# Performance work log

Measured on AMD Instinct MI355X. Metric: run time of the kernel, lower is better.

Reference implementation:

```python
import jax, jax.numpy as jnp
import numpy as np

N, E, G, T, H, ED, IN_D, OUT_D = 50000, 1600000, 64, 5, 64, 9, 10, 3
EPS = 1e-6

def _seg_mean(vals, seg, num):
    s = jax.ops.segment_sum(vals, seg, num_segments=num)
    c = jax.ops.segment_sum(jnp.ones((vals.shape[0],), vals.dtype), seg, num_segments=num)
    return s / jnp.maximum(c, 1.0)[:, None], c

def per_graph_edge_norm(edge_attr, edge_graph, num_graphs):
    # standardize each edge-feature column per graph (zero-shot transfer trick)
    mu, _ = _seg_mean(edge_attr, edge_graph, num_graphs)
    sq, _ = _seg_mean(edge_attr * edge_attr, edge_graph, num_graphs)
    var = jnp.maximum(sq - mu * mu, 0.0)
    std = jnp.sqrt(var)
    return (edge_attr - mu[edge_graph]) / (std[edge_graph] + EPS)

def setup_inputs() -> dict:
    key = jax.random.key(0)
    ks = jax.random.split(key, 24)
    s = 0.05  # weight scale to keep ReLU chains stable
    inp = {
        'x': jax.random.normal(ks[0], (N, IN_D), jnp.float32),
        'edge_index': jax.random.randint(ks[1], (2, E), 0, N),
        'edge_attr': jax.random.normal(ks[2], (E, ED), jnp.float32),
        'batch': jnp.sort(jax.random.randint(ks[3], (N,), 0, G)),
        'lift_W1': jax.random.normal(ks[4], (IN_D, H), jnp.float32) * s,
        'lift_b1': jnp.zeros((H,), jnp.float32),
        'lift_W2': jax.random.normal(ks[5], (H, H), jnp.float32) * s,
        'lift_b2': jnp.zeros((H,), jnp.float32),
        'Wself': jax.random.normal(ks[6], (T, H, H), jnp.float32) * s,
        'bself': jnp.zeros((T, H), jnp.float32),
        'msg_W0': jax.random.normal(ks[7], (T, H + ED, H), jnp.float32) * s,
        'msg_b0': jnp.zeros((T, H), jnp.float32),
        'msg_W1': jax.random.normal(ks[8], (T, H, H), jnp.float32) * s,
        'msg_b1': jnp.zeros((T, H), jnp.float32),
        'msg_W2': jax.random.normal(ks[9], (T, H, H), jnp.float32) * s,
        'msg_b2': jnp.zeros((T, H), jnp.float32),
        'gate_W': jax.random.normal(ks[10], (T, 1, H), jnp.float32) * s,
        'gate_b': jnp.zeros((T, H), jnp.float32),
        'proj_W1': jax.random.normal(ks[11], (H, H), jnp.float32) * s,
        'proj_b1': jnp.zeros((H,), jnp.float32),
        'proj_W2': jax.random.normal(ks[12], (H, OUT_D), jnp.float32) * s,
        'proj_b2': jnp.zeros((OUT_D,), jnp.float32),
    }
    return inp

def _gno(x, edge_index, edge_attr, batch,
         lift_W1, lift_b1, lift_W2, lift_b2,
         Wself, bself, msg_W0, msg_b0, msg_W1, msg_b1, msg_W2, msg_b2,
         gate_W, gate_b, proj_W1, proj_b1, proj_W2, proj_b2):
    src, dst = edge_index[0], edge_index[1]
    edge_graph = batch[src]
    ea = per_graph_edge_norm(edge_attr, edge_graph, G)  # cols 0:9 == all cols
    log_diag_y = x[:, 4:5]                               # [N,1]
    v0 = jax.nn.relu(x @ lift_W1 + lift_b1) @ lift_W2 + lift_b2  # lift
    v = v0
    for t in range(T):
        # gather -> per-edge MLP -> scatter-mean (AdmittanceKernelLayer)
        h = jnp.concatenate([v[src], ea], axis=-1)              # [E, H+ED]
        h = jax.nn.relu(h @ msg_W0[t] + msg_b0[t])
        h = jax.nn.relu(h @ msg_W1[t] + msg_b1[t])
        m = h @ msg_W2[t] + msg_b2[t]                           # [E, H]
        agg, _ = _seg_mean(m, dst, N)                           # mean aggregation
        gate = jax.nn.sigmoid(log_diag_y @ gate_W[t] + gate_b[t])  # [N,H]
        v = jax.nn.relu(v @ Wself[t] + bself[t] + agg + v0) * gate
        # dropout inactive at inference
    out = jax.nn.relu(v @ proj_W1 + proj_b1) @ proj_W2 + proj_b2  # project
    return out

def reference(x, edge_index, edge_attr, batch,
              lift_W1, lift_b1, lift_W2, lift_b2,
              Wself, bself, msg_W0, msg_b0, msg_W1, msg_b1, msg_W2, msg_b2,
              gate_W, gate_b, proj_W1, proj_b1, proj_W2, proj_b2):
    return _gno(x, edge_index, edge_attr, batch,
                lift_W1, lift_b1, lift_W2, lift_b2,
                Wself, bself, msg_W0, msg_b0, msg_W1, msg_b1, msg_W2, msg_b2,
                gate_W, gate_b, proj_W1, proj_b1, proj_W2, proj_b2)
```

## Files before the change

### kernel.cpp

```cpp
#include <hip/hip_runtime.h>
#include <math.h>

#define NN 50000
#define NE 1600000
#define NG 64
#define NT 5
#define NH 64
#define NED 9
#define NIN 10
#define NOUT 3
#define EPSF 1e-6f
#define NSUB (NE / 16)

typedef __attribute__((ext_vector_type(8))) short s8v;
typedef __attribute__((ext_vector_type(4))) short s4v;
typedef __attribute__((ext_vector_type(4))) float f32x4;

__device__ __forceinline__ unsigned short f2bf(float f) {
    union { float f; unsigned int u; } v; v.f = f;
    unsigned int r = v.u + 0x7FFFu + ((v.u >> 16) & 1u);
    return (unsigned short)(r >> 16);
}
__device__ __forceinline__ float bf2f(unsigned short b) {
    union { unsigned int u; float f; } v; v.u = ((unsigned int)b) << 16;
    return v.f;
}

__global__ void stats_kernel(const int* __restrict__ ei, const float* __restrict__ ea,
                             const int* __restrict__ batch,
                             float* __restrict__ ssum, float* __restrict__ ssq,
                             float* __restrict__ scnt, int* __restrict__ ecnt) {
    __shared__ float lsum[NG * NED];
    __shared__ float lsq[NG * NED];
    __shared__ float lcnt[NG];
    for (int i = threadIdx.x; i < NG * NED; i += blockDim.x) { lsum[i] = 0.f; lsq[i] = 0.f; }
    for (int i = threadIdx.x; i < NG; i += blockDim.x) lcnt[i] = 0.f;
    __syncthreads();
    int lane = threadIdx.x & 63;
    int stride = gridDim.x * blockDim.x;
    for (int e = blockIdx.x * blockDim.x + threadIdx.x; e < NE; e += stride) {
        int s = ei[e];
        int g = batch[s];
        atomicAdd(&ecnt[ei[NE + e]], 1);
        float a[NED];
#pragma unroll
        for (int d = 0; d < NED; ++d) a[d] = ea[(size_t)e * NED + d];
        int g0 = __builtin_amdgcn_readfirstlane(g);
        if (__all(g == g0)) {
            float sv[NED], qv[NED];
#pragma unroll
            for (int d = 0; d < NED; ++d) { sv[d] = a[d]; qv[d] = a[d] * a[d]; }
#pragma unroll
            for (int off = 32; off; off >>= 1) {
#pragma unroll
                for (int d = 0; d < NED; ++d) {
                    sv[d] += __shfl_down(sv[d], off);
                    qv[d] += __shfl_down(qv[d], off);
                }
            }
            if (lane == 0) {
#pragma unroll
                for (int d = 0; d < NED; ++d) {
                    atomicAdd(&lsum[g0 * NED + d], sv[d]);
                    atomicAdd(&lsq[g0 * NED + d], qv[d]);
                }
                atomicAdd(&lcnt[g0], 64.f);
            }
        } else {
            atomicAdd(&lcnt[g], 1.0f);
#pragma unroll
            for (int d = 0; d < NED; ++d) {
                atomicAdd(&lsum[g * NED + d], a[d]);
                atomicAdd(&lsq[g * NED + d], a[d] * a[d]);
            }
        }
    }
    __syncthreads();
    for (int i = threadIdx.x; i < NG * NED; i += blockDim.x) {
        atomicAdd(&ssum[i], lsum[i]);
        atomicAdd(&ssq[i], lsq[i]);
    }
    for (int i = threadIdx.x; i < NG; i += blockDim.x) atomicAdd(&scnt[i], lcnt[i]);
}

__global__ void stats_fin(const float* __restrict__ ssum, const float* __restrict__ ssq,
                          const float* __restrict__ scnt,
                          float* __restrict__ mu, float* __restrict__ rstd) {
    int i = blockIdx.x * blockDim.x + threadIdx.x;
    if (i >= NG * NED) return;
    int g = i / NED;
    float c = fmaxf(scnt[g], 1.0f);
    float m = ssum[i] / c;
    float q = ssq[i] / c;
    float var = fmaxf(q - m * m, 0.f);
    mu[i] = m;
    rstd[i] = 1.0f / (sqrtf(var) + EPSF);
}

__global__ void scan1_kernel(const int* __restrict__ ecnt, int* __restrict__ partial) {
    __shared__ int sm[256];
    int i = blockIdx.x * 256 + threadIdx.x;
    sm[threadIdx.x] = (i < NN) ? ecnt[i] : 0;
    __syncthreads();
    for (int off = 128; off; off >>= 1) {
        if (threadIdx.x < off) sm[threadIdx.x] += sm[threadIdx.x + off];
        __syncthreads();
    }
    if (threadIdx.x == 0) partial[blockIdx.x] = sm[0];
}
__global__ void scan2_kernel(int* __restrict__ partial, int nb) {
    __shared__ int sm[256];
    int t = threadIdx.x;
    sm[t] = (t < nb) ? partial[t] : 0;
    __syncthreads();
    for (int off = 1; off < 256; off <<= 1) {
        int v = (t >= off) ? sm[t - off] : 0;
        __syncthreads();
        sm[t] += v;
        __syncthreads();
    }
    if (t < nb) partial[t] = (t ? sm[t - 1] : 0);
}
__global__ void scan3_kernel(const int* __restrict__ ecnt, const int* __restrict__ partial,
                             int* __restrict__ offs) {
    __shared__ int sm[256];
    int b = blockIdx.x, t = threadIdx.x, i = b * 256 + t;
    int x = (i < NN) ? ecnt[i] : 0;
    sm[t] = x;
    __syncthreads();
    for (int off = 1; off < 256; off <<= 1) {
        int v = (t >= off) ? sm[t - off] : 0;
        __syncthreads();
        sm[t] += v;
        __syncthreads();
    }
    if (i < NN) offs[i] = sm[t] - x + partial[b];
}

__global__ void permute_kernel(const int* __restrict__ ei, const int* __restrict__ offs,
                               int* __restrict__ cursor, int* __restrict__ perm) {
    int stride = gridDim.x * blockDim.x;
    for (int e = blockIdx.x * blockDim.x + threadIdx.x; e < NE; e += stride) {
        int d = ei[NE + e];
        int pos = offs[d] + atomicAdd(&cursor[d], 1);
        perm[pos] = e;
    }
}

__global__ void pack_kernel(const int* __restrict__ perm, const int* __restrict__ ei,
                            const float* __restrict__ ea, const int* __restrict__ batch,
                            const float* __restrict__ mu, const float* __restrict__ rstd,
                            int* __restrict__ srcPerm, int* __restrict__ dstPerm,
                            unsigned short* __restrict__ eaN) {
    int stride = gridDim.x * blockDim.x;
    for (int p = blockIdx.x * blockDim.x + threadIdx.x; p < NE; p += stride) {
        int e = perm[p];
        int s = ei[e], d = ei[NE + e];
        int g = batch[s];
        srcPerm[p] = s;
        dstPerm[p] = d;
#pragma unroll
        for (int k = 0; k < NED; ++k) {
            float val = (ea[(size_t)e * NED + k] - mu[g * NED + k]) * rstd[g * NED + k];
            eaN[(size_t)k * NE + p] = f2bf(val);
        }
    }
}

__global__ __launch_bounds__(256) void lift_kernel(
    const float* __restrict__ x,
    const float* __restrict__ W1, const float* __restrict__ b1,
    const float* __restrict__ W2, const float* __restrict__ b2,
    float* __restrict__ v0, float* __restrict__ v, float* __restrict__ ldy) {
    __shared__ float sW1[NIN * NH];
    __shared__ __align__(16) float sW2[NH][NH];
    __shared__ float sb1[NH], sb2[NH];
    for (int i = threadIdx.x; i < NIN * NH; i += blockDim.x) sW1[i] = W1[i];
    for (int i = threadIdx.x; i < NH * NH; i += blockDim.x) {
        int k = i >> 6, j = i & 63;
        sW2[j][k] = W2[i];
    }
    for (int i = threadIdx.x; i < NH; i += blockDim.x) { sb1[i] = b1[i]; sb2[i] = b2[i]; }
    __syncthreads();
    int stride = gridDim.x * blockDim.x;
    for (int n = blockIdx.x * blockDim.x + threadIdx.x; n < NN; n += stride) {
        float xr[NIN];
#pragma unroll
        for (int k = 0; k < NIN; ++k) xr[k] = x[(size_t)n * NIN + k];
        ldy[n] = xr[4];
        float h[NH];
#pragma unroll
        for (int j = 0; j < NH; ++j) {
            float acc = sb1[j];
#pragma unroll
            for (int k = 0; k < NIN; ++k) acc += xr[k] * sW1[k * NH + j];
            h[j] = fmaxf(acc, 0.f);
        }
#pragma unroll
        for (int j = 0; j < NH; ++j) {
            float acc = sb2[j];
#pragma unroll
            for (int k = 0; k < NH; k += 4) {
                float4 w = *(const float4*)&sW2[j][k];
                acc += h[k] * w.x + h[k + 1] * w.y + h[k + 2] * w.z + h[k + 3] * w.w;
            }
            v0[(size_t)n * NH + j] = acc;
            v[(size_t)n * NH + j] = acc;
        }
    }
}

__device__ __forceinline__ void gemm_acc68(const float* __restrict__ Ab,
                                           const float* __restrict__ Wb,
                                           int K, int te, int tj, float acc[4][4]) {
#pragma unroll 4
    for (int k = 0; k < K; ++k) {
        float4 a = *(const float4*)(Ab + k * 68 + (te << 2));
        float4 b = *(const float4*)(Wb + (k << 6) + (tj << 2));
        acc[0][0] = fmaf(a.x, b.x, acc[0][0]);
        acc[0][1] = fmaf(a.x, b.y, acc[0][1]);
        acc[0][2] = fmaf(a.x, b.z, acc[0][2]);
        acc[0][3] = fmaf(a.x, b.w, acc[0][3]);
        acc[1][0] = fmaf(a.y, b.x, acc[1][0]);
        acc[1][1] = fmaf(a.y, b.y, acc[1][1]);
        acc[1][2] = fmaf(a.y, b.z, acc[1][2]);
        acc[1][3] = fmaf(a.y, b.w, acc[1][3]);
        acc[2][0] = fmaf(a.z, b.x, acc[2][0]);
        acc[2][1] = fmaf(a.z, b.y, acc[2][1]);
        acc[2][2] = fmaf(a.z, b.z, acc[2][2]);
        acc[2][3] = fmaf(a.z, b.w, acc[2][3]);
        acc[3][0] = fmaf(a.w, b.x, acc[3][0]);
        acc[3][1] = fmaf(a.w, b.y, acc[3][1]);
        acc[3][2] = fmaf(a.w, b.z, acc[3][2]);
        acc[3][3] = fmaf(a.w, b.w, acc[3][3]);
    }
}

__global__ __launch_bounds__(256, 4) void u_kernel(
    const float* __restrict__ v, const float* __restrict__ W0v,
    const float* __restrict__ b0, float* __restrict__ U) {
    __shared__ __align__(16) float Vt[64][68];
    __shared__ __align__(16) float sW[64][64];
    __shared__ float sb[64];
    const int tid = threadIdx.x;
    const int base = blockIdx.x * 64;
    const int te = tid >> 4, tj = tid & 15;

    {
        int r = tid >> 2;
        int kb = (tid & 3) << 4;
        int n = base + r;
        const float4* vrow = (const float4*)(v + (size_t)n * NH + kb);
#pragma unroll
        for (int q = 0; q < 4; ++q) {
            float4 f = (n < NN) ? vrow[q] : make_float4(0.f, 0.f, 0.f, 0.f);
            int k = kb + q * 4;
            Vt[k + 0][r] = f.x; Vt[k + 1][r] = f.y; Vt[k + 2][r] = f.z; Vt[k + 3][r] = f.w;
        }
    }
    for (int i4 = tid; i4 < 64 * 16; i4 += 256) {
        int k = i4 >> 4, c4 = i4 & 15;
        *(float4*)&sW[k][c4 * 4] = *(const float4*)(W0v + (size_t)k * 64 + c4 * 4);
    }
    if (tid < 64) sb[tid] = b0[tid];
    __syncthreads();

    float acc[4][4];
    {
        float b0_ = sb[tj * 4 + 0], b1_ = sb[tj * 4 + 1], b2_ = sb[tj * 4 + 2], b3_ = sb[tj * 4 + 3];
#pragma unroll
        for (int ee = 0; ee < 4; ++ee) { acc[ee][0] = b0_; acc[ee][1] = b1_; acc[ee][2] = b2_; acc[ee][3] = b3_; }
    }
    gemm_acc68(&Vt[0][0], &sW[0][0], 64, te, tj, acc);

#pragma unroll
    for (int ee = 0; ee < 4; ++ee) {
        int n = base + te * 4 + ee;
        if (n < NN)
            *(float4*)&U[(size_t)n * NH + tj * 4] =
                make_float4(acc[ee][0], acc[ee][1], acc[ee][2], acc[ee][3]);
    }
}

__global__ __launch_bounds__(256, 4) void edge4_kernel(
    const int* __restrict__ srcPerm, const int* __restrict__ dstPerm,
    const unsigned short* __restrict__ eaN,
    const float* __restrict__ W0e, const float* __restrict__ W1, const float* __restrict__ b1,
    const float* __restrict__ U, float* __restrict__ nodesum) {
    __shared__ __align__(16) float sWe[NED][64];
    __shared__ __align__(16) short W1frag[8][64][8];
    __shared__ __align__(16) short h0bf[4][16 * 64];
    __shared__ __align__(16) float h1s[4][16 * 64];
    __shared__ int sDstS[4][16];

    const int tid = threadIdx.x;
    const int lane = tid & 63, w = tid >> 6;
    const int l15 = lane & 15, l4 = lane >> 4;

    for (int i4 = tid; i4 < NED * 16; i4 += 256) {
        int k = i4 >> 4, c4 = i4 & 15;
        *(float4*)&sWe[k][c4 * 4] = *(const float4*)(W0e + (size_t)k * 64 + c4 * 4);
    }
    for (int idx = tid; idx < 2 * 4 * 64; idx += 256) {
        int kc = idx >> 8, c = (idx >> 6) & 3, ln = idx & 63;
        int fl15 = ln & 15, fl4 = ln >> 4;
        int col = 16 * c + fl15;
        s8v frag;
#pragma unroll
        for (int j = 0; j < 8; ++j) {
            int k = kc * 32 + fl4 * 8 + j;
            frag[j] = (short)f2bf(W1[(size_t)k * 64 + col]);
        }
        *(s8v*)&W1frag[kc * 4 + c][ln][0] = frag;
    }
    float b1r[4];
#pragma unroll
    for (int c = 0; c < 4; ++c) b1r[c] = b1[16 * c + l15];
    __syncthreads();

    short* myh0 = h0bf[w];
    float* myh1 = h1s[w];
    int*   myd  = sDstS[w];
    const int gw = blockIdx.x * 4 + w;
    const int nw = gridDim.x * 4;

    for (int st = gw; st < NSUB; st += nw) {
        const int e16 = st * 16;
        if (lane < 16) myd[lane] = dstPerm[e16 + lane];

        int4 s4 = *(const int4*)(srcPerm + e16 + 4 * l4);
        ushort4 eu[NED];
#pragma unroll
        for (int d = 0; d < NED; ++d)
            eu[d] = *(const ushort4*)(eaN + (size_t)d * NE + e16 + 4 * l4);

        float acc0[4][4];
        {
            const int* sp = (const int*)&s4;
#pragma unroll
            for (int ee = 0; ee < 4; ++ee) {
                float4 u4 = *(const float4*)(U + (size_t)sp[ee] * NH + 4 * l15);
                acc0[ee][0] = u4.x; acc0[ee][1] = u4.y; acc0[ee][2] = u4.z; acc0[ee][3] = u4.w;
            }
        }
#pragma unroll
        for (int d = 0; d < NED; ++d) {
            float4 wv = *(const float4*)&sWe[d][4 * l15];
            float a0 = bf2f((unsigned short)eu[d].x), a1 = bf2f((unsigned short)eu[d].y);
            float a2 = bf2f((unsigned short)eu[d].z), a3 = bf2f((unsigned short)eu[d].w);
            acc0[0][0] = fmaf(a0, wv.x, acc0[0][0]); acc0[0][1] = fmaf(a0, wv.y, acc0[0][1]);
            acc0[0][2] = fmaf(a0, wv.z, acc0[0][2]); acc0[0][3] = fmaf(a0, wv.w, acc0[0][3]);
            acc0[1][0] = fmaf(a1, wv.x, acc0[1][0]); acc0[1][1] = fmaf(a1, wv.y, acc0[1][1]);
            acc0[1][2] = fmaf(a1, wv.z, acc0[1][2]); acc0[1][3] = fmaf(a1, wv.w, acc0[1][3]);
            acc0[2][0] = fmaf(a2, wv.x, acc0[2][0]); acc0[2][1] = fmaf(a2, wv.y, acc0[2][1]);
            acc0[2][2] = fmaf(a2, wv.z, acc0[2][2]); acc0[2][3] = fmaf(a2, wv.w, acc0[2][3]);
            acc0[3][0] = fmaf(a3, wv.x, acc0[3][0]); acc0[3][1] = fmaf(a3, wv.y, acc0[3][1]);
            acc0[3][2] = fmaf(a3, wv.z, acc0[3][2]); acc0[3][3] = fmaf(a3, wv.w, acc0[3][3]);
        }

#pragma unroll
        for (int ee = 0; ee < 4; ++ee) {
            int row = 4 * l4 + ee;
            s4v p;
            p[0] = (short)f2bf(fmaxf(acc0[ee][0], 0.f));
            p[1] = (short)f2bf(fmaxf(acc0[ee][1], 0.f));
            p[2] = (short)f2bf(fmaxf(acc0[ee][2], 0.f));
            p[3] = (short)f2bf(fmaxf(acc0[ee][3], 0.f));
            *(s4v*)((char*)myh0 + row * 128 + ((l15 * 8) ^ ((row & 7) << 4))) = p;
        }

        f32x4 acc[4];
#pragma unroll
        for (int c = 0; c < 4; ++c) {
            float b = b1r[c];
            acc[c][0] = b; acc[c][1] = b; acc[c][2] = b; acc[c][3] = b;
        }
        {
            const char* abase = (const char*)myh0 + l15 * 128;
            const int aswz = (l15 & 7) << 4;
#pragma unroll
            for (int kc = 0; kc < 2; ++kc) {
                s8v af = *(const s8v*)(abase + ((l4 * 16 + kc * 64) ^ aswz));
#pragma unroll
                for (int c = 0; c < 4; ++c) {
                    s8v bf = *(const s8v*)&W1frag[kc * 4 + c][lane][0];
                    acc[c] = __builtin_amdgcn_mfma_f32_16x16x32_bf16(af, bf, acc[c], 0, 0, 0);
                }
            }
        }

        int dFirst = myd[0];
        int dLast = myd[15];
        if (dFirst == dLast) {
#pragma unroll
            for (int c = 0; c < 4; ++c) {
                float vs = fmaxf(acc[c][0], 0.f) + fmaxf(acc[c][1], 0.f) +
                           fmaxf(acc[c][2], 0.f) + fmaxf(acc[c][3], 0.f);
                vs += __shfl_xor(vs, 16);
                vs += __shfl_xor(vs, 32);
                if (l4 == 0)
                    atomicAdd(&nodesum[(size_t)dFirst * NH + 16 * c + l15], vs);
            }
        } else {
#pragma unroll
            for (int r = 0; r < 4; ++r) {
                int row = 4 * l4 + r;
#pragma unroll
                for (int c = 0; c < 4; ++c)
                    myh1[row * 64 + ((16 * c + l15) ^ (l4 * 8))] = fmaxf(acc[c][r], 0.f);
            }
            int cur = dFirst;
            float a = myh1[lane];
#pragma unroll
            for (int i = 1; i < 16; ++i) {
                int dn = myd[i];
                float hv = myh1[i * 64 + (lane ^ ((i >> 2) * 8))];
                if (dn != cur) {
                    atomicAdd(&nodesum[(size_t)cur * NH + lane], a);
                    cur = dn;
                    a = hv;
                } else {
                    a += hv;
                }
            }
            atomicAdd(&nodesum[(size_t)cur * NH + lane], a);
        }
    }
}

__global__ __launch_bounds__(256, 2) void update3_kernel(
    const float* __restrict__ Wself, const float* __restrict__ bself,
    const float* __restrict__ W2, const float* __restrict__ b2,
    const float* __restrict__ gWt, const float* __restrict__ gbt,
    const float* __restrict__ v0, const float* __restrict__ ldy,
    const int* __restrict__ ecnt, const float* __restrict__ nodesum,
    float* __restrict__ v) {
    __shared__ __align__(16) float Vt[64][68];
    __shared__ __align__(16) float St[64][68];
    __shared__ __align__(16) float sWs[64][64];
    __shared__ __align__(16) float sW2[64][64];
    __shared__ float sbs[64], sb2[64], sgw[64], sgb[64];
    const int tid = threadIdx.x;
    const int base = blockIdx.x * 64;
    const int te = tid >> 4, tj = tid & 15;

    {
        int r = tid >> 2;
        int kb = (tid & 3) << 4;
        int n = base + r;
        const float4* vrow = (const float4*)(v + (size_t)n * NH + kb);
        const float4* srow = (const float4*)(nodesum + (size_t)n * NH + kb);
#pragma unroll
        for (int q = 0; q < 4; ++q) {
            float4 f = (n < NN) ? vrow[q] : make_float4(0.f, 0.f, 0.f, 0.f);
            float4 g = (n < NN) ? srow[q] : make_float4(0.f, 0.f, 0.f, 0.f);
            int k = kb + q * 4;
            Vt[k + 0][r] = f.x; Vt[k + 1][r] = f.y; Vt[k + 2][r] = f.z; Vt[k + 3][r] = f.w;
            St[k + 0][r] = g.x; St[k + 1][r] = g.y; St[k + 2][r] = g.z; St[k + 3][r] = g.w;
        }
    }
    for (int i4 = tid; i4 < 64 * 16; i4 += 256) {
        int k = i4 >> 4, c4 = i4 & 15;
        *(float4*)&sWs[k][c4 * 4] = *(const float4*)(Wself + (size_t)k * 64 + c4 * 4);
        *(float4*)&sW2[k][c4 * 4] = *(const float4*)(W2 + (size_t)k * 64 + c4 * 4);
    }
    if (tid < 64) { sbs[tid] = bself[tid]; sb2[tid] = b2[tid]; sgw[tid] = gWt[tid]; sgb[tid] = gbt[tid]; }
    __syncthreads();

    float acc1[4][4], acc2[4][4];
    {
        float b0_ = sbs[tj * 4 + 0], b1_ = sbs[tj * 4 + 1], b2_ = sbs[tj * 4 + 2], b3_ = sbs[tj * 4 + 3];
#pragma unroll
        for (int ee = 0; ee < 4; ++ee) {
            acc1[ee][0] = b0_; acc1[ee][1] = b1_; acc1[ee][2] = b2_; acc1[ee][3] = b3_;
            acc2[ee][0] = 0.f; acc2[ee][1] = 0.f; acc2[ee][2] = 0.f; acc2[ee][3] = 0.f;
        }
    }
    gemm_acc68(&Vt[0][0], &sWs[0][0], 64, te, tj, acc1);
    gemm_acc68(&St[0][0], &sW2[0][0], 64, te, tj, acc2);

    float gw0 = sgw[tj * 4 + 0], gw1 = sgw[tj * 4 + 1], gw2 = sgw[tj * 4 + 2], gw3 = sgw[tj * 4 + 3];
    float gb0 = sgb[tj * 4 + 0], gb1 = sgb[tj * 4 + 1], gb2 = sgb[tj * 4 + 2], gb3 = sgb[tj * 4 + 3];
    float bb0 = sb2[tj * 4 + 0], bb1 = sb2[tj * 4 + 1], bb2 = sb2[tj * 4 + 2], bb3 = sb2[tj * 4 + 3];
#pragma unroll
    for (int ee = 0; ee < 4; ++ee) {
        int n = base + te * 4 + ee;
        if (n >= NN) continue;
        float cnt = (float)ecnt[n];
        float has = (cnt > 0.5f) ? 1.f : 0.f;
        float dninv = has / fmaxf(cnt, 1.f);
        float ld = ldy[n];
        float4 v0r = *(const float4*)&v0[(size_t)n * NH + tj * 4];
        float z0 = acc1[ee][0] + acc2[ee][0] * dninv + bb0 * has + v0r.x;
        float z1 = acc1[ee][1] + acc2[ee][1] * dninv + bb1 * has + v0r.y;
        float z2 = acc1[ee][2] + acc2[ee][2] * dninv + bb2 * has + v0r.z;
        float z3 = acc1[ee][3] + acc2[ee][3] * dninv + bb3 * has + v0r.w;
        float g0 = 1.f / (1.f + expf(-(ld * gw0 + gb0)));
        float g1 = 1.f / (1.f + expf(-(ld * gw1 + gb1)));
        float g2 = 1.f / (1.f + expf(-(ld * gw2 + gb2)));
        float g3 = 1.f / (1.f + expf(-(ld * gw3 + gb3)));
        *(float4*)&v[(size_t)n * NH + tj * 4] =
            make_float4(fmaxf(z0, 0.f) * g0, fmaxf(z1, 0.f) * g1,
                        fmaxf(z2, 0.f) * g2, fmaxf(z3, 0.f) * g3);
    }
}

__global__ __launch_bounds__(256) void proj_kernel(
    const float* __restrict__ v,
    const float* __restrict__ pW1, const float* __restrict__ pb1,
    const float* __restrict__ pW2, const float* __restrict__ pb2,
    float* __restrict__ out) {
    __shared__ __align__(16) float sW1[NH][NH];
    __shared__ float sb1[NH];
    __shared__ float sW2[NH * NOUT];
    __shared__ float sb2[NOUT];
    for (int i = threadIdx.x; i < NH * NH; i += blockDim.x) {
        int k = i >> 6, j = i & 63;
        sW1[j][k] = pW1[i];
    }
    for (int i = threadIdx.x; i < NH; i += blockDim.x) sb1[i] = pb1[i];
    for (int i = threadIdx.x; i < NH * NOUT; i += blockDim.x) sW2[i] = pW2[i];
    for (int i = threadIdx.x; i < NOUT; i += blockDim.x) sb2[i] = pb2[i];
    __syncthreads();
    int stride = gridDim.x * blockDim.x;
    for (int n = blockIdx.x * blockDim.x + threadIdx.x; n < NN; n += stride) {
        float vr[NH];
        const float4* vp = (const float4*)(v + (size_t)n * NH);
#pragma unroll
        for (int q = 0; q < NH / 4; ++q) {
            float4 f = vp[q];
            vr[4 * q + 0] = f.x; vr[4 * q + 1] = f.y; vr[4 * q + 2] = f.z; vr[4 * q + 3] = f.w;
        }
        float o0 = sb2[0], o1 = sb2[1], o2 = sb2[2];
#pragma unroll
        for (int j = 0; j < NH; ++j) {
            float acc = sb1[j];
#pragma unroll
            for (int k = 0; k < NH; k += 4) {
                float4 w = *(const float4*)&sW1[j][k];
                acc += vr[k] * w.x + vr[k + 1] * w.y + vr[k + 2] * w.z + vr[k + 3] * w.w;
            }
            float h = fmaxf(acc, 0.f);
            o0 += h * sW2[j * NOUT + 0];
            o1 += h * sW2[j * NOUT + 1];
            o2 += h * sW2[j * NOUT + 2];
        }
        out[(size_t)n * NOUT + 0] = o0;
        out[(size_t)n * NOUT + 1] = o1;
        out[(size_t)n * NOUT + 2] = o2;
    }
}

extern "C" void kernel_launch(void* const* d_in, const int* in_sizes, int n_in,
                              void* d_out, int out_size, void* d_ws, size_t ws_size,
                              hipStream_t stream) {
    (void)in_sizes; (void)n_in; (void)out_size; (void)ws_size;
    const float* x     = (const float*)d_in[0];
    const int*   ei    = (const int*)d_in[1];
    const float* ea    = (const float*)d_in[2];
    const int*   batch = (const int*)d_in[3];
    const float* lW1   = (const float*)d_in[4];
    const float* lb1   = (const float*)d_in[5];
    const float* lW2   = (const float*)d_in[6];
    const float* lb2   = (const float*)d_in[7];
    const float* Wself = (const float*)d_in[8];
    const float* bself = (const float*)d_in[9];
    const float* mW0   = (const float*)d_in[10];
    const float* mb0   = (const float*)d_in[11];
    const float* mW1   = (const float*)d_in[12];
    const float* mb1   = (const float*)d_in[13];
    const float* mW2   = (const float*)d_in[14];
    const float* mb2   = (const float*)d_in[15];
    const float* gW    = (const float*)d_in[16];
    const float* gb    = (const float*)d_in[17];
    const float* pW1   = (const float*)d_in[18];
    const float* pb1   = (const float*)d_in[19];
    const float* pW2   = (const float*)d_in[20];
    const float* pb2   = (const float*)d_in[21];
    float* out = (float*)d_out;
    float* ws  = (float*)d_ws;

    float* nodesum = ws;
    float* v0   = nodesum + (size_t)NN * NH;
    float* v    = v0 + (size_t)NN * NH;
    float* U    = v + (size_t)NN * NH;
    float* ldy  = U + (size_t)NN * NH;
    float* mu   = ldy + NN;
    float* rstd = mu + NG * NED;
    float* ssum = rstd + NG * NED;
    float* ssq  = ssum + NG * NED;
    float* scnt = ssq + NG * NED;
    int*   ecnt   = (int*)(scnt + NG);
    int*   cursor = ecnt + NN;
    int*   offs    = cursor + NN;
    int*   partial = offs + NN;
    int*   srcPerm = partial + 256;
    int*   dstPerm = srcPerm + NE;
    unsigned short* eaN = (unsigned short*)(dstPerm + NE);
    int*   perm = (int*)nodesum;

    const int NBLK = (NN + 63) / 64;
    const int SBLK = (NN + 255) / 256;

    hipMemsetAsync(ssum, 0, ((size_t)(2 * NG * NED + NG) + 2 * NN) * sizeof(float), stream);

    stats_kernel<<<512, 256, 0, stream>>>(ei, ea, batch, ssum, ssq, scnt, ecnt);
    stats_fin<<<3, 256, 0, stream>>>(ssum, ssq, scnt, mu, rstd);
    scan1_kernel<<<SBLK, 256, 0, stream>>>(ecnt, partial);
    scan2_kernel<<<1, 256, 0, stream>>>(partial, SBLK);
    scan3_kernel<<<SBLK, 256, 0, stream>>>(ecnt, partial, offs);
    permute_kernel<<<2048, 256, 0, stream>>>(ei, offs, cursor, perm);
    pack_kernel<<<2048, 256, 0, stream>>>(perm, ei, ea, batch, mu, rstd, srcPerm, dstPerm, eaN);
    lift_kernel<<<200, 256, 0, stream>>>(x, lW1, lb1, lW2, lb2, v0, v, ldy);

    for (int t = 0; t < NT; ++t) {
        const float* W0t = mW0 + (size_t)t * (NH + NED) * NH;
        hipMemsetAsync(nodesum, 0, (size_t)NN * NH * sizeof(float), stream);
        u_kernel<<<NBLK, 256, 0, stream>>>(v, W0t, mb0 + (size_t)t * NH, U);
        edge4_kernel<<<1024, 256, 0, stream>>>(
            srcPerm, dstPerm, eaN,
            W0t + (size_t)NH * NH,
            mW1 + (size_t)t * NH * NH, mb1 + (size_t)t * NH,
            U, nodesum);
        update3_kernel<<<NBLK, 256, 0, stream>>>(
            Wself + (size_t)t * NH * NH, bself + (size_t)t * NH,
            mW2 + (size_t)t * NH * NH, mb2 + (size_t)t * NH,
            gW + (size_t)t * NH, gb + (size_t)t * NH,
            v0, ldy, ecnt, nodesum, v);
    }
    proj_kernel<<<200, 256, 0, stream>>>(v, pW1, pb1, pW2, pb2, out);
}
```

Measured before the change: 1.370 ms.

## Reduce edge-kernel scatter in registers, drop h1 LDS buffer, raise occupancy

Replaces the LDS-staged segmented reduction of per-edge messages with an in-register path. When each 16-edge tile spans only two destination nodes, it uses shuffle-reduced sums. Otherwise each lane runs a segmented sum over its 4 rows. Removing the 16 KB h1 shared buffer lets launch bounds rise to 6 blocks/SM and the grid to double. The fallback path issues more atomics per tile, and the higher occupancy target may cause register spills.

Result: slower. 2.391 ms (+74.5%).

```diff
diff --git a/kernel.cpp b/kernel.cpp
--- a/kernel.cpp
+++ b/kernel.cpp
@@ -282,7 +282,7 @@
     }
 }
 
-__global__ __launch_bounds__(256, 4) void edge4_kernel(
+__global__ __launch_bounds__(256, 6) void edge4_kernel(
     const int* __restrict__ srcPerm, const int* __restrict__ dstPerm,
     const unsigned short* __restrict__ eaN,
     const float* __restrict__ W0e, const float* __restrict__ W1, const float* __restrict__ b1,
@@ -290,7 +290,6 @@
     __shared__ __align__(16) float sWe[NED][64];
     __shared__ __align__(16) short W1frag[8][64][8];
     __shared__ __align__(16) short h0bf[4][16 * 64];
-    __shared__ __align__(16) float h1s[4][16 * 64];
     __shared__ int sDstS[4][16];
 
     const int tid = threadIdx.x;
@@ -319,7 +318,6 @@
     __syncthreads();
 
     short* myh0 = h0bf[w];
-    float* myh1 = h1s[w];
     int*   myd  = sDstS[w];
     const int gw = blockIdx.x * 4 + w;
     const int nw = gridDim.x * 4;
@@ -402,28 +400,46 @@
                     atomicAdd(&nodesum[(size_t)dFirst * NH + 16 * c + l15], vs);
             }
         } else {
-#pragma unroll
-            for (int r = 0; r < 4; ++r) {
-                int row = 4 * l4 + r;
-#pragma unroll
-                for (int c = 0; c < 4; ++c)
-                    myh1[row * 64 + ((16 * c + l15) ^ (l4 * 8))] = fmaxf(acc[c][r], 0.f);
-            }
-            int cur = dFirst;
-            float a = myh1[lane];
-#pragma unroll
-            for (int i = 1; i < 16; ++i) {
-                int dn = myd[i];
-                float hv = myh1[i * 64 + (lane ^ ((i >> 2) * 8))];
-                if (dn != cur) {
-                    atomicAdd(&nodesum[(size_t)cur * NH + lane], a);
-                    cur = dn;
-                    a = hv;
-                } else {
-                    a += hv;
+            int dr[4];
+#pragma unroll
+            for (int r = 0; r < 4; ++r) dr[r] = myd[4 * l4 + r];
+            bool two = (dr[0] == dFirst || dr[0] == dLast) &&
+                       (dr[1] == dFirst || dr[1] == dLast) &&
+                       (dr[2] == dFirst || dr[2] == dLast) &&
+                       (dr[3] == dFirst || dr[3] == dLast);
+            if (__all(two)) {
+#pragma unroll
+                for (int c = 0; c < 4; ++c) {
+                    float sa = 0.f, sb = 0.f;
+#pragma unroll
+                    for (int r = 0; r < 4; ++r) {
+                        float hv = fmaxf(acc[c][r], 0.f);
+                        if (dr[r] == dFirst) sa += hv; else sb += hv;
+                    }
+                    sa += __shfl_xor(sa, 16); sa += __shfl_xor(sa, 32);
+                    sb += __shfl_xor(sb, 16); sb += __shfl_xor(sb, 32);
+                    if (l4 == 0) atomicAdd(&nodesum[(size_t)dFirst * NH + 16 * c + l15], sa);
+                    if (l4 == 1) atomicAdd(&nodesum[(size_t)dLast * NH + 16 * c + l15], sb);
                 }
-            }
-            atomicAdd(&nodesum[(size_t)cur * NH + lane], a);
+            } else {
+#pragma unroll
+                for (int c = 0; c < 4; ++c) {
+                    float run = fmaxf(acc[c][0], 0.f);
+                    int cur = dr[0];
+#pragma unroll
+                    for (int r = 1; r < 4; ++r) {
+                        float hv = fmaxf(acc[c][r], 0.f);
+                        if (dr[r] != cur) {
+                            atomicAdd(&nodesum[(size_t)cur * NH + 16 * c + l15], run);
+                            cur = dr[r];
+                            run = hv;
+                        } else {
+                            run += hv;
+                        }
+                    }
+                    atomicAdd(&nodesum[(size_t)cur * NH + 16 * c + l15], run);
+                }
+            }
         }
     }
 }
@@ -617,7 +633,7 @@
         const float* W0t = mW0 + (size_t)t * (NH + NED) * NH;
         hipMemsetAsync(nodesum, 0, (size_t)NN * NH * sizeof(float), stream);
         u_kernel<<<NBLK, 256, 0, stream>>>(v, W0t, mb0 + (size_t)t * NH, U);
-        edge4_kernel<<<1024, 256, 0, stream>>>(
+        edge4_kernel<<<2048, 256, 0, stream>>>(
             srcPerm, dstPerm, eaN,
             W0t + (size_t)NH * NH,
             mW1 + (size_t)t * NH * NH, mb1 + (size_t)t * NH,
```
